# Optimization experiments

Hardware: AMD Instinct MI355X
Metric: run time of the kernel (lower is better)

The kernel has to match this reference:

```python
import jax, jax.numpy as jnp
import numpy as np

H = 8
D = 512
DK = D // H  # 64
ALPHA = 0.2  # leaky relu negative slope


def setup_inputs() -> dict:
    key = jax.random.key(0)
    ks = jax.random.split(key, 10)
    B, N = 8, 1024
    query = jax.random.normal(ks[0], (B, N, D), dtype=jnp.float32)
    key_t = jax.random.normal(ks[1], (B, N, D), dtype=jnp.float32)
    value = jax.random.normal(ks[2], (B, N, D), dtype=jnp.float32)
    mask = jax.random.randint(ks[3], (B, N, N), 0, 2, dtype=jnp.int32)
    scale = 0.02
    Wq = jax.random.normal(ks[4], (D, D), dtype=jnp.float32) * scale
    Wk = jax.random.normal(ks[5], (D, D), dtype=jnp.float32) * scale
    Wv = jax.random.normal(ks[6], (D, D), dtype=jnp.float32) * scale
    Wo = jax.random.normal(ks[7], (D, D), dtype=jnp.float32) * scale
    bq = jnp.zeros((D,), jnp.float32)
    bk = jnp.zeros((D,), jnp.float32)
    bv = jnp.zeros((D,), jnp.float32)
    bo = jnp.zeros((D,), jnp.float32)
    # xavier-uniform-like init for the attention vector a: shape (h, 2*d_k)
    limit = float(np.sqrt(6.0 / (H + 2 * DK)))
    a = jax.random.uniform(ks[8], (H, 2 * DK), dtype=jnp.float32, minval=-limit, maxval=limit)
    return {"query": query, "key": key_t, "value": value, "mask": mask,
            "Wq": Wq, "bq": bq, "Wk": Wk, "bk": bk, "Wv": Wv, "bv": bv,
            "Wo": Wo, "bo": bo, "a": a}


def reference(query, key, value, mask, Wq, bq, Wk, bk, Wv, bv, Wo, bo, a):
    B, N, _ = query.shape

    def proj(x, W, b):
        # torch Linear: x @ W.T + b, then split heads -> (B, H, N, DK)
        return (x @ W.T + b).reshape(B, N, H, DK).transpose(0, 2, 1, 3)

    q = proj(query, Wq, bq)
    k = proj(key, Wk, bk)
    v = proj(value, Wv, bv)

    # 'cat' attention: scores[b,h,i,j] = concat(q_i, k_j) . a[h]
    #                = q_i . a[h,:DK] + k_j . a[h,DK:]  (algebraic decomposition,
    #                 avoids the O(N^2 * 2*DK) concat tensor of the torch code)
    sq = jnp.einsum('bhnd,hd->bhn', q, a[:, :DK])
    sk = jnp.einsum('bhnd,hd->bhn', k, a[:, DK:])
    scores = sq[:, :, :, None] + sk[:, :, None, :]  # (B, H, N, N)

    # mask == 0 -> -inf (mask broadcast over heads), applied BEFORE leaky relu
    scores = jnp.where(mask[:, None, :, :] == 0, -jnp.inf, scores)
    # leaky relu (leaky_relu(-inf) == -inf, preserved)
    scores = jnp.where(scores >= 0, scores, ALPHA * scores)

    p = jax.nn.softmax(scores, axis=-1)
    # fully-masked rows produce NaN -> replace with 0 (as in the torch code)
    p = jnp.where(jnp.isnan(p), jnp.zeros_like(p), p)

    x = jnp.einsum('bhnm,bhmd->bhnd', p, v)
    x = x.transpose(0, 2, 1, 3).reshape(B, N, D)
    return x @ Wo.T + bo
```

## Files before the change

### kernel.cpp

```cpp
#include <hip/hip_runtime.h>
#include <hip/hip_bf16.h>
#include <stdint.h>


typedef __attribute__((ext_vector_type(8))) short short8;
typedef __attribute__((ext_vector_type(4))) float f32x4;

#define LB __launch_bounds__(256)

union U8 { unsigned u[4]; short8 s; uint4 v; };
union U2 { unsigned u[2]; uint2 v; };

__device__ __forceinline__ unsigned short f2bf(float f) {
  unsigned int u = __float_as_uint(f);
  u += 0x7fffu + ((u >> 16) & 1u);
  return (unsigned short)(u >> 16);
}

__device__ __forceinline__ unsigned cvt_pk(float a, float b) {
  unsigned r;
  asm("v_cvt_pk_bf16_f32 %0, %1, %2" : "=v"(r) : "v"(a), "v"(b));
  return r;
}

__device__ __forceinline__ void async_cp16(const void* g, void* l) {
  __builtin_amdgcn_global_load_lds(
      (const __attribute__((address_space(1))) unsigned int*)g,
      (__attribute__((address_space(3))) unsigned int*)l, 16, 0, 0);
}

__global__ LB void prep_kernel(const int* __restrict__ mask, unsigned int* __restrict__ bits,
                               const float* __restrict__ value, unsigned short* __restrict__ vb,
                               const float* __restrict__ Wv, const float* __restrict__ Wo,
                               unsigned short* __restrict__ wv16, unsigned short* __restrict__ wo16,
                               const float* __restrict__ Wq, const float* __restrict__ Wk,
                               const float* __restrict__ a, const float* __restrict__ bq,
                               const float* __restrict__ bk,
                               unsigned short* __restrict__ Bfrag, float* __restrict__ qkb) {
  const int blk = blockIdx.x;
  if (blk < 32768) {
    const size_t idx = (size_t)blk * 256 + threadIdx.x;
    const unsigned long long bl = __ballot(mask[idx] != 0);
    if ((threadIdx.x & 63) == 0) {
      bits[idx >> 5] = (unsigned int)bl;
      bits[(idx >> 5) + 1] = (unsigned int)(bl >> 32);
    }
    return;
  }
  if (blk < 36864) {
    const int idx = ((blk - 32768) * 256 + threadIdx.x) * 4;
    const float4 v = *(const float4*)(value + idx);
    U2 pk;
    pk.u[0] = cvt_pk(v.x, v.y);
    pk.u[1] = cvt_pk(v.z, v.w);
    *(uint2*)(vb + idx) = pk.v;
    return;
  }
  if (blk < 37376) {
    const int wblk = blk - 36864;
    const float* src = wblk < 256 ? Wv : Wo;
    unsigned short* dst = wblk < 256 ? wv16 : wo16;
    const int idx = ((wblk & 255) * 256 + threadIdx.x) * 4;
    const float4 v = *(const float4*)(src + idx);
    U2 pk;
    pk.u[0] = cvt_pk(v.x, v.y);
    pk.u[1] = cvt_pk(v.z, v.w);
    *(uint2*)(dst + idx) = pk.v;
    return;
  }
  const int t = (blk - 37376) * 256 + threadIdx.x;
  const int d = t & 511, h = t >> 9;
  float aq = 0.f, ak = 0.f;
#pragma unroll 4
  for (int dk = 0; dk < 64; ++dk) {
    aq += Wq[(size_t)(h * 64 + dk) * 512 + d] * a[h * 128 + dk];
    ak += Wk[(size_t)(h * 64 + dk) * 512 + d] * a[h * 128 + 64 + dk];
  }
  const float L2E = 1.4426950408889634f;
  const int ks = d >> 5, lch = (d >> 3) & 3, tt = d & 7;
  Bfrag[((ks * 64 + (lch << 4) + h) << 3) + tt] = f2bf(aq * L2E);
  Bfrag[((ks * 64 + (lch << 4) + 8 + h) << 3) + tt] = f2bf(ak * L2E);
  if (d == 0) {
    float s1 = 0.f, s2 = 0.f;
    for (int dk = 0; dk < 64; ++dk) {
      s1 += bq[h * 64 + dk] * a[h * 128 + dk];
      s2 += bk[h * 64 + dk] * a[h * 128 + 64 + dk];
    }
    qkb[h] = s1 * L2E;
    qkb[8 + h] = s2 * L2E;
  }
}

__global__ LB void sqsk_kernel(const float* __restrict__ query, const float* __restrict__ key,
                               const unsigned short* __restrict__ Bfrag,
                               const float* __restrict__ qkb,
                               float* __restrict__ sq, float* __restrict__ sk) {
  __shared__ float comb[3 * 64 * 9];
  const int tid = threadIdx.x, wv = tid >> 6, l = tid & 63;
  const int m0 = blockIdx.x * 16;
  const int k0 = wv * 128;
  short8 bf[4];
#pragma unroll
  for (int ks = 0; ks < 4; ++ks)
    bf[ks] = *(const short8*)(Bfrag + (((wv * 4 + ks) * 64 + l) << 3));
  const float* qbase = query + (size_t)(m0 + (l & 15)) * 512 + k0 + ((l >> 4) << 3);
  const float* kbase = key + (size_t)(m0 + (l & 15)) * 512 + k0 + ((l >> 4) << 3);
  f32x4 cq = {}, ck = {};
#pragma unroll
  for (int ks = 0; ks < 4; ++ks) {
    const float4 q0 = *(const float4*)(qbase + ks * 32);
    const float4 q1 = *(const float4*)(qbase + ks * 32 + 4);
    const float4 k0v = *(const float4*)(kbase + ks * 32);
    const float4 k1v = *(const float4*)(kbase + ks * 32 + 4);
    U8 aq, ak;
    aq.u[0] = cvt_pk(q0.x, q0.y); aq.u[1] = cvt_pk(q0.z, q0.w);
    aq.u[2] = cvt_pk(q1.x, q1.y); aq.u[3] = cvt_pk(q1.z, q1.w);
    ak.u[0] = cvt_pk(k0v.x, k0v.y); ak.u[1] = cvt_pk(k0v.z, k0v.w);
    ak.u[2] = cvt_pk(k1v.x, k1v.y); ak.u[3] = cvt_pk(k1v.z, k1v.w);
    cq = __builtin_amdgcn_mfma_f32_16x16x32_bf16(aq.s, bf[ks], cq, 0, 0, 0);
    ck = __builtin_amdgcn_mfma_f32_16x16x32_bf16(ak.s, bf[ks], ck, 0, 0, 0);
  }
  if (wv) {
    float* p = comb + ((wv - 1) * 64 + l) * 9;
#pragma unroll
    for (int r = 0; r < 4; ++r) { p[r] = cq[r]; p[4 + r] = ck[r]; }
  }
  __syncthreads();
  if (wv == 0) {
#pragma unroll
    for (int j = 0; j < 3; ++j) {
      const float* p = comb + (j * 64 + l) * 9;
#pragma unroll
      for (int r = 0; r < 4; ++r) { cq[r] += p[r]; ck[r] += p[4 + r]; }
    }
    const int col = l & 15;
    const int mbase = m0 + ((l >> 4) << 2);
    const int b = mbase >> 10;
    const float bia = qkb[col];
    if (col < 8) {
      float* out = sq + ((size_t)b * 8 + col) * 1024;
#pragma unroll
      for (int r = 0; r < 4; ++r) out[(mbase + r) & 1023] = cq[r] + bia;
    } else {
      float* out = sk + ((size_t)b * 8 + (col - 8)) * 1024;
#pragma unroll
      for (int r = 0; r < 4; ++r) out[(mbase + r) & 1023] = ck[r] + bia;
    }
  }
}

template <int BB16, int MODE>
__global__ LB void gemm_bt(const unsigned short* __restrict__ A,
                           const void* __restrict__ Bwp,
                           const float* __restrict__ bias, void* __restrict__ outp) {
  __shared__ unsigned short As[2][32 * 32];
  __shared__ unsigned short Bs[2][128 * 32];
  const int tid = threadIdx.x;
  const int w = tid >> 6, l = tid & 63;
  const int lr = l & 15, lc = l >> 4;
  const int bm = blockIdx.x >> 2, bn = blockIdx.x & 3;
  const int m0 = bm * 32, n0 = bn * 128;
  const int wr = (w & 1) * 16, wc = (w >> 1) * 64;
  const int rch = (lc ^ ((lr >> 1) & 3)) << 3;
  const int arow = (w << 3) + (l >> 2);
  const int asc = (l & 3) ^ ((arow >> 1) & 3);
  const unsigned short* asrc = A + (size_t)(m0 + arow) * 512 + (asc << 3);
  const int crow = l >> 2;
  const unsigned short* b16 = (const unsigned short*)Bwp;
  const float* b32 = (const float*)Bwp;
  const int brow0 = (w << 4) + crow, brow1 = ((w + 4) << 4) + crow;
  const unsigned short* bsrc0 = b16 + (size_t)(n0 + brow0) * 512 + (((l & 3) ^ ((brow0 >> 1) & 3)) << 3);
  const unsigned short* bsrc1 = b16 + (size_t)(n0 + brow1) * 512 + (((l & 3) ^ ((brow1 >> 1) & 3)) << 3);

  f32x4 acc[4] = {};
  if (BB16) {
    if (l < 32) async_cp16(asrc, As[0] + (w << 8));
    async_cp16(bsrc0, Bs[0] + (w << 9));
    async_cp16(bsrc1, Bs[0] + ((w + 4) << 9));
    int buf = 0;
    for (int kt = 0; kt < 16; ++kt) {
      if (kt < 15) {
        const int k1 = (kt + 1) * 32;
        if (l < 32) async_cp16(asrc + k1, As[buf ^ 1] + (w << 8));
        async_cp16(bsrc0 + k1, Bs[buf ^ 1] + (w << 9));
        async_cp16(bsrc1 + k1, Bs[buf ^ 1] + ((w + 4) << 9));
        asm volatile("s_waitcnt vmcnt(3)" ::: "memory");
      } else {
        asm volatile("s_waitcnt vmcnt(0)" ::: "memory");
      }
      __builtin_amdgcn_sched_barrier(0);
      __builtin_amdgcn_s_barrier();
      const short8 af = *(const short8*)(As[buf] + (wr + lr) * 32 + rch);
      __builtin_amdgcn_s_setprio(1);
#pragma unroll
      for (int j = 0; j < 4; ++j) {
        const short8 bfr = *(const short8*)(Bs[buf] + (wc + j * 16 + lr) * 32 + rch);
        acc[j] = __builtin_amdgcn_mfma_f32_16x16x32_bf16(af, bfr, acc[j], 0, 0, 0);
      }
      __builtin_amdgcn_s_setprio(0);
      if (kt < 15) __builtin_amdgcn_s_barrier();
      buf ^= 1;
    }
  } else {
    for (int kt = 0; kt < 16; ++kt) {
      const int k0 = kt * 32;
      if (kt) __syncthreads();
      if (l < 32) async_cp16(asrc + k0, As[0] + (w << 8));
#pragma unroll
      for (int it = 0; it < 2; ++it) {
        const int idx = it * 256 + tid;
        const int row = idx >> 2, gr = idx & 3;
        const int sch = (gr ^ ((row >> 1) & 3)) << 3;
        const float4* src = (const float4*)(b32 + (size_t)(n0 + row) * 512 + k0 + gr * 8);
        const float4 b0 = src[0], b1 = src[1];
        U8 t8;
        t8.u[0] = cvt_pk(b0.x, b0.y); t8.u[1] = cvt_pk(b0.z, b0.w);
        t8.u[2] = cvt_pk(b1.x, b1.y); t8.u[3] = cvt_pk(b1.z, b1.w);
        *(uint4*)(Bs[0] + row * 32 + sch) = t8.v;
      }
      __syncthreads();
      const short8 af = *(const short8*)(As[0] + (wr + lr) * 32 + rch);
#pragma unroll
      for (int j = 0; j < 4; ++j) {
        const short8 bfr = *(const short8*)(Bs[0] + (wc + j * 16 + lr) * 32 + rch);
        acc[j] = __builtin_amdgcn_mfma_f32_16x16x32_bf16(af, bfr, acc[j], 0, 0, 0);
      }
    }
  }
#pragma unroll
  for (int j = 0; j < 4; ++j) {
    const int nn = n0 + wc + j * 16 + lr;
    const float bia = bias[nn];
    const int mm0 = m0 + wr + lc * 4;
    if (MODE == 0) {
      float* out = (float*)outp;
#pragma unroll
      for (int r = 0; r < 4; ++r)
        out[(size_t)(mm0 + r) * 512 + nn] = acc[j][r] + bia;
    } else {
      unsigned short* out = (unsigned short*)outp;
      const int b = mm0 >> 10, t0 = mm0 & 1023;
      const int h = nn >> 6, dk = nn & 63;
      U2 pk;
      pk.u[0] = cvt_pk(acc[j][0] + bia, acc[j][1] + bia);
      pk.u[1] = cvt_pk(acc[j][2] + bia, acc[j][3] + bia);
      *(uint2*)(out + (((size_t)((b * 8 + h) * 64 + dk)) << 10) + t0) = pk.v;
    }
  }
}

__global__ LB void attn_kernel(const float* __restrict__ sq, const float* __restrict__ sk,
                               const unsigned char* __restrict__ mbits,
                               const unsigned short* __restrict__ vt,
                               unsigned short* __restrict__ xb) {
  __shared__ char smem[28672];
  unsigned short* vts = (unsigned short*)smem;
  float* sks = (float*)(smem + 16384);
  char* mks = smem + 20480;
  const int tid = threadIdx.x;
  const int w = tid >> 6, l = tid & 63;
  const int lr = l & 15, lc = l >> 4;
  const int bid = blockIdx.x;
  const int bh = bid >> 4, iblk = bid & 15;
  const int b = bh >> 3, h = bh & 7;
  const int i0b = iblk * 64;
  const float* sqp = sq + (size_t)bh * 1024;
  const float* skp = sk + (size_t)bh * 1024;
  const unsigned short* vtp = vt + ((size_t)bh << 16);
  const unsigned char* mrow = mbits + ((size_t)b << 17);

  async_cp16(skp + (w << 8) + l * 4, sks + (w << 8));
#pragma unroll
  for (int m = 0; m < 2; ++m) {
    const int row = (w << 4) + (m << 3) + (l >> 3);
    const int c = (l & 7) ^ (row & 7);
    async_cp16(mrow + (size_t)(i0b + row) * 128 + (c << 4), mks + (w << 11) + (m << 10));
  }
  const int strow = (w << 4) + (l >> 2);
  const int stc = (l & 3) ^ ((strow >> 1) & 3);
  const unsigned short* srcw = vtp + strow * 1024 + (stc << 3);
  async_cp16(srcw, vts + (w << 9));
  async_cp16(srcw + 32, vts + 2048 + (w << 9));

  const int rowl = (w << 4) + lr;
  const float sq1 = sqp[i0b + rowl];
  __syncthreads();

  f32x4 acc[4] = {};
  f32x4 accs = {};
  short8 ones;
#pragma unroll
  for (int t = 0; t < 8; ++t) ones[t] = (short)0x3f80;
  const int mrowbase = rowl << 7;
  const int rxorb = (rowl & 7) << 4;
  const int vread = (lc ^ ((lr >> 1) & 3)) << 3;

  int bufp = 0;
  for (int it = 0; it < 16; ++it) {
    if (it < 15) {
      const int sl = (it + 1) << 1;
      unsigned short* dst = vts + ((bufp ^ 1) << 12) + (w << 9);
      async_cp16(srcw + sl * 32, dst);
      async_cp16(srcw + sl * 32 + 32, dst + 2048);
      asm volatile("s_waitcnt vmcnt(2)" ::: "memory");
    } else {
      asm volatile("s_waitcnt vmcnt(0)" ::: "memory");
    }
    __builtin_amdgcn_sched_barrier(0);
    __builtin_amdgcn_s_barrier();
#pragma unroll
    for (int sub = 0; sub < 2; ++sub) {
      const int jb = (it << 6) + (sub << 5);
      const unsigned int mb = (unsigned char)mks[mrowbase + (((jb >> 3) + lc) ^ rxorb)];
      const f32x4 s0 = *(const f32x4*)(sks + jb + (lc << 3));
      const f32x4 s1 = *(const f32x4*)(sks + jb + (lc << 3) + 4);
      float e[8];
#pragma unroll
      for (int t = 0; t < 8; ++t) {
        float s = sq1 + (t < 4 ? s0[t] : s1[t - 4]);
        s = fmaxf(s, 0.2f * s);
        const float ex = __builtin_amdgcn_exp2f(s);
        e[t] = (mb & (1u << t)) ? ex : 0.0f;
      }
      U8 pa;
      pa.u[0] = cvt_pk(e[0], e[1]); pa.u[1] = cvt_pk(e[2], e[3]);
      pa.u[2] = cvt_pk(e[4], e[5]); pa.u[3] = cvt_pk(e[6], e[7]);
      const unsigned short* vb_base = vts + (bufp << 12) + (sub << 11) + vread;
      __builtin_amdgcn_s_setprio(1);
#pragma unroll
      for (int c = 0; c < 4; ++c) {
        const short8 bv = *(const short8*)(vb_base + ((c << 4) + lr) * 32);
        acc[c] = __builtin_amdgcn_mfma_f32_16x16x32_bf16(pa.s, bv, acc[c], 0, 0, 0);
      }
      accs = __builtin_amdgcn_mfma_f32_16x16x32_bf16(pa.s, ones, accs, 0, 0, 0);
      __builtin_amdgcn_s_setprio(0);
    }
    if (it < 15) __builtin_amdgcn_s_barrier();
    bufp ^= 1;
  }

#pragma unroll
  for (int r = 0; r < 4; ++r) {
    const float s = accs[r];
    const float inv = s > 0.0f ? 1.0f / s : 0.0f;
    const int i = i0b + (w << 4) + lc * 4 + r;
#pragma unroll
    for (int c = 0; c < 4; ++c)
      xb[(((size_t)(b * 1024 + i)) << 9) + h * 64 + c * 16 + lr] =
          f2bf(acc[c][r] * inv);
  }
}

extern "C" void kernel_launch(void* const* d_in, const int* in_sizes, int n_in,
                              void* d_out, int out_size, void* d_ws, size_t ws_size,
                              hipStream_t stream) {
  const float* query = (const float*)d_in[0];
  const float* key   = (const float*)d_in[1];
  const float* value = (const float*)d_in[2];
  const int*   mask  = (const int*)d_in[3];
  const float* Wq = (const float*)d_in[4];
  const float* bq = (const float*)d_in[5];
  const float* Wk = (const float*)d_in[6];
  const float* bk = (const float*)d_in[7];
  const float* Wv = (const float*)d_in[8];
  const float* bv = (const float*)d_in[9];
  const float* Wo = (const float*)d_in[10];
  const float* bo = (const float*)d_in[11];
  const float* a  = (const float*)d_in[12];

  char* oc = (char*)d_out;
  unsigned short* vt = (unsigned short*)(oc + 0);
  unsigned int* mbits = (unsigned int*)(oc + 8388608);
  float* sqv = (float*)(oc + 9437184);
  float* skv = (float*)(oc + 9699328);
  unsigned short* Bfrag = (unsigned short*)(oc + 9961472);
  float* qkb = (float*)(oc + 9977856);
  unsigned short* wv16 = (unsigned short*)(oc + 10485760);
  unsigned short* wo16f = (unsigned short*)(oc + 11010048);
  unsigned short* vb = (unsigned short*)d_ws;
  unsigned short* xb = (unsigned short*)d_ws;

  const bool roomy = ws_size >= 8912896;
  unsigned short* wo16 = roomy ? (unsigned short*)((char*)d_ws + 8388608) : wo16f;

  prep_kernel<<<37392, 256, 0, stream>>>(mask, mbits, value, vb, Wv, Wo, wv16, wo16,
                                         Wq, Wk, a, bq, bk, Bfrag, qkb);
  sqsk_kernel<<<512, 256, 0, stream>>>(query, key, Bfrag, qkb, sqv, skv);
  gemm_bt<1, 1><<<1024, 256, 0, stream>>>(vb, (const void*)wv16, bv, (void*)vt);
  attn_kernel<<<1024, 256, 0, stream>>>(sqv, skv, (const unsigned char*)mbits, vt, xb);
  if (roomy)
    gemm_bt<1, 0><<<1024, 256, 0, stream>>>(xb, (const void*)wo16, bo, d_out);
  else
    gemm_bt<0, 0><<<1024, 256, 0, stream>>>(xb, (const void*)Wo, bo, d_out);
}
```

Before: 90.43 us.

## Vectorize mask packing, merge sqsk with V GEMM, double attention row tile

The mask bit-packing now has each thread read four ints with one vector load and builds the bit words through shared memory, so it needs a quarter of the blocks. The sq/sk projection kernel and the V projection GEMM are merged into one launch with disjoint block ranges, removing a kernel launch and letting the two run concurrently. The attention kernel now handles 128 query rows per block instead of 64, with two row groups per wave, so each staged V tile is reused twice. This halves the attention grid and raises LDS use, which may reduce occupancy.

```diff
diff --git a/kernel.cpp b/kernel.cpp
--- a/kernel.cpp
+++ b/kernel.cpp
@@ -37,18 +37,24 @@
                                const float* __restrict__ a, const float* __restrict__ bq,
                                const float* __restrict__ bk,
                                unsigned short* __restrict__ Bfrag, float* __restrict__ qkb) {
-  const int blk = blockIdx.x;
-  if (blk < 32768) {
-    const size_t idx = (size_t)blk * 256 + threadIdx.x;
-    const unsigned long long bl = __ballot(mask[idx] != 0);
-    if ((threadIdx.x & 63) == 0) {
-      bits[idx >> 5] = (unsigned int)bl;
-      bits[(idx >> 5) + 1] = (unsigned int)(bl >> 32);
+  const int blk = blockIdx.x, tid = threadIdx.x;
+  if (blk < 8192) {
+    __shared__ unsigned char nb[256];
+    const size_t e0 = ((size_t)blk * 256 + tid) * 4;
+    const int4 m = *(const int4*)(mask + e0);
+    nb[tid] = (unsigned char)((m.x != 0) | ((m.y != 0) << 1) | ((m.z != 0) << 2) | ((m.w != 0) << 3));
+    __syncthreads();
+    if (tid < 32) {
+      const uint2 p = *(const uint2*)(nb + tid * 8);
+      const unsigned lo = p.x, hi = p.y;
+      const unsigned wl = (lo & 0xFu) | ((lo >> 4) & 0xF0u) | ((lo >> 8) & 0xF00u) | ((lo >> 12) & 0xF000u);
+      const unsigned wh = (hi & 0xFu) | ((hi >> 4) & 0xF0u) | ((hi >> 8) & 0xF00u) | ((hi >> 12) & 0xF000u);
+      bits[blk * 32 + tid] = wl | (wh << 16);
     }
     return;
   }
-  if (blk < 36864) {
-    const int idx = ((blk - 32768) * 256 + threadIdx.x) * 4;
+  if (blk < 12288) {
+    const int idx = ((blk - 8192) * 256 + tid) * 4;
     const float4 v = *(const float4*)(value + idx);
     U2 pk;
     pk.u[0] = cvt_pk(v.x, v.y);
@@ -56,11 +62,11 @@
     *(uint2*)(vb + idx) = pk.v;
     return;
   }
-  if (blk < 37376) {
-    const int wblk = blk - 36864;
+  if (blk < 12800) {
+    const int wblk = blk - 12288;
     const float* src = wblk < 256 ? Wv : Wo;
     unsigned short* dst = wblk < 256 ? wv16 : wo16;
-    const int idx = ((wblk & 255) * 256 + threadIdx.x) * 4;
+    const int idx = ((wblk & 255) * 256 + tid) * 4;
     const float4 v = *(const float4*)(src + idx);
     U2 pk;
     pk.u[0] = cvt_pk(v.x, v.y);
@@ -68,7 +74,7 @@
     *(uint2*)(dst + idx) = pk.v;
     return;
   }
-  const int t = (blk - 37376) * 256 + threadIdx.x;
+  const int t = (blk - 12800) * 256 + tid;
   const int d = t & 511, h = t >> 9;
   float aq = 0.f, ak = 0.f;
 #pragma unroll 4
@@ -91,61 +97,124 @@
   }
 }
 
-__global__ LB void sqsk_kernel(const float* __restrict__ query, const float* __restrict__ key,
-                               const unsigned short* __restrict__ Bfrag,
-                               const float* __restrict__ qkb,
-                               float* __restrict__ sq, float* __restrict__ sk) {
-  __shared__ float comb[3 * 64 * 9];
-  const int tid = threadIdx.x, wv = tid >> 6, l = tid & 63;
-  const int m0 = blockIdx.x * 16;
-  const int k0 = wv * 128;
-  short8 bf[4];
-#pragma unroll
-  for (int ks = 0; ks < 4; ++ks)
-    bf[ks] = *(const short8*)(Bfrag + (((wv * 4 + ks) * 64 + l) << 3));
-  const float* qbase = query + (size_t)(m0 + (l & 15)) * 512 + k0 + ((l >> 4) << 3);
-  const float* kbase = key + (size_t)(m0 + (l & 15)) * 512 + k0 + ((l >> 4) << 3);
-  f32x4 cq = {}, ck = {};
-#pragma unroll
-  for (int ks = 0; ks < 4; ++ks) {
-    const float4 q0 = *(const float4*)(qbase + ks * 32);
-    const float4 q1 = *(const float4*)(qbase + ks * 32 + 4);
-    const float4 k0v = *(const float4*)(kbase + ks * 32);
-    const float4 k1v = *(const float4*)(kbase + ks * 32 + 4);
-    U8 aq, ak;
-    aq.u[0] = cvt_pk(q0.x, q0.y); aq.u[1] = cvt_pk(q0.z, q0.w);
-    aq.u[2] = cvt_pk(q1.x, q1.y); aq.u[3] = cvt_pk(q1.z, q1.w);
-    ak.u[0] = cvt_pk(k0v.x, k0v.y); ak.u[1] = cvt_pk(k0v.z, k0v.w);
-    ak.u[2] = cvt_pk(k1v.x, k1v.y); ak.u[3] = cvt_pk(k1v.z, k1v.w);
-    cq = __builtin_amdgcn_mfma_f32_16x16x32_bf16(aq.s, bf[ks], cq, 0, 0, 0);
-    ck = __builtin_amdgcn_mfma_f32_16x16x32_bf16(ak.s, bf[ks], ck, 0, 0, 0);
-  }
-  if (wv) {
-    float* p = comb + ((wv - 1) * 64 + l) * 9;
-#pragma unroll
-    for (int r = 0; r < 4; ++r) { p[r] = cq[r]; p[4 + r] = ck[r]; }
-  }
-  __syncthreads();
-  if (wv == 0) {
-#pragma unroll
-    for (int j = 0; j < 3; ++j) {
-      const float* p = comb + (j * 64 + l) * 9;
-#pragma unroll
-      for (int r = 0; r < 4; ++r) { cq[r] += p[r]; ck[r] += p[4 + r]; }
-    }
-    const int col = l & 15;
-    const int mbase = m0 + ((l >> 4) << 2);
-    const int b = mbase >> 10;
-    const float bia = qkb[col];
-    if (col < 8) {
-      float* out = sq + ((size_t)b * 8 + col) * 1024;
-#pragma unroll
-      for (int r = 0; r < 4; ++r) out[(mbase + r) & 1023] = cq[r] + bia;
+__global__ LB void sqsk_gemmv_kernel(const float* __restrict__ query, const float* __restrict__ key,
+                                     const unsigned short* __restrict__ Bfrag,
+                                     const float* __restrict__ qkb,
+                                     float* __restrict__ sq, float* __restrict__ sk,
+                                     const unsigned short* __restrict__ vbA,
+                                     const unsigned short* __restrict__ wv16,
+                                     const float* __restrict__ bvb,
+                                     unsigned short* __restrict__ vt) {
+  __shared__ char sm[20480];
+  const int tid = threadIdx.x, w = tid >> 6, l = tid & 63;
+  const int lr = l & 15, lc = l >> 4;
+  if (blockIdx.x < 512) {
+    float* comb = (float*)sm;
+    const int m0 = blockIdx.x * 16;
+    const int k0 = w * 128;
+    short8 bf[4];
+#pragma unroll
+    for (int ks = 0; ks < 4; ++ks)
+      bf[ks] = *(const short8*)(Bfrag + (((w * 4 + ks) * 64 + l) << 3));
+    const float* qbase = query + (size_t)(m0 + lr) * 512 + k0 + (lc << 3);
+    const float* kbase = key + (size_t)(m0 + lr) * 512 + k0 + (lc << 3);
+    f32x4 cq = {}, ck = {};
+#pragma unroll
+    for (int ks = 0; ks < 4; ++ks) {
+      const float4 q0 = *(const float4*)(qbase + ks * 32);
+      const float4 q1 = *(const float4*)(qbase + ks * 32 + 4);
+      const float4 k0v = *(const float4*)(kbase + ks * 32);
+      const float4 k1v = *(const float4*)(kbase + ks * 32 + 4);
+      U8 aq, ak;
+      aq.u[0] = cvt_pk(q0.x, q0.y); aq.u[1] = cvt_pk(q0.z, q0.w);
+      aq.u[2] = cvt_pk(q1.x, q1.y); aq.u[3] = cvt_pk(q1.z, q1.w);
+      ak.u[0] = cvt_pk(k0v.x, k0v.y); ak.u[1] = cvt_pk(k0v.z, k0v.w);
+      ak.u[2] = cvt_pk(k1v.x, k1v.y); ak.u[3] = cvt_pk(k1v.z, k1v.w);
+      cq = __builtin_amdgcn_mfma_f32_16x16x32_bf16(aq.s, bf[ks], cq, 0, 0, 0);
+      ck = __builtin_amdgcn_mfma_f32_16x16x32_bf16(ak.s, bf[ks], ck, 0, 0, 0);
+    }
+    if (w) {
+      float* p = comb + ((w - 1) * 64 + l) * 9;
+#pragma unroll
+      for (int r = 0; r < 4; ++r) { p[r] = cq[r]; p[4 + r] = ck[r]; }
+    }
+    __syncthreads();
+    if (w == 0) {
+#pragma unroll
+      for (int j = 0; j < 3; ++j) {
+        const float* p = comb + (j * 64 + l) * 9;
+#pragma unroll
+        for (int r = 0; r < 4; ++r) { cq[r] += p[r]; ck[r] += p[4 + r]; }
+      }
+      const int col = l & 15;
+      const int mbase = m0 + (lc << 2);
+      const int b = mbase >> 10;
+      const float bia = qkb[col];
+      if (col < 8) {
+        float* out = sq + ((size_t)b * 8 + col) * 1024;
+#pragma unroll
+        for (int r = 0; r < 4; ++r) out[(mbase + r) & 1023] = cq[r] + bia;
+      } else {
+        float* out = sk + ((size_t)b * 8 + (col - 8)) * 1024;
+#pragma unroll
+        for (int r = 0; r < 4; ++r) out[(mbase + r) & 1023] = ck[r] + bia;
+      }
+    }
+    return;
+  }
+  unsigned short* As = (unsigned short*)sm;
+  unsigned short* Bs = (unsigned short*)(sm + 4096);
+  const int bid = blockIdx.x - 512;
+  const int bm = bid >> 2, bn = bid & 3;
+  const int m0 = bm * 32, n0 = bn * 128;
+  const int wr = (w & 1) * 16, wc = (w >> 1) * 64;
+  const int rch = (lc ^ ((lr >> 1) & 3)) << 3;
+  const int arow = (w << 3) + (l >> 2);
+  const int asc = (l & 3) ^ ((arow >> 1) & 3);
+  const unsigned short* asrc = vbA + (size_t)(m0 + arow) * 512 + (asc << 3);
+  const int crow = l >> 2;
+  const int brow0 = (w << 4) + crow, brow1 = ((w + 4) << 4) + crow;
+  const unsigned short* bsrc0 = wv16 + (size_t)(n0 + brow0) * 512 + (((l & 3) ^ ((brow0 >> 1) & 3)) << 3);
+  const unsigned short* bsrc1 = wv16 + (size_t)(n0 + brow1) * 512 + (((l & 3) ^ ((brow1 >> 1) & 3)) << 3);
+  f32x4 acc[4] = {};
+  if (l < 32) async_cp16(asrc, As + (w << 8));
+  async_cp16(bsrc0, Bs + (w << 9));
+  async_cp16(bsrc1, Bs + ((w + 4) << 9));
+  int buf = 0;
+  for (int kt = 0; kt < 16; ++kt) {
+    if (kt < 15) {
+      const int k1 = (kt + 1) * 32;
+      if (l < 32) async_cp16(asrc + k1, As + ((buf ^ 1) << 10) + (w << 8));
+      async_cp16(bsrc0 + k1, Bs + ((buf ^ 1) << 12) + (w << 9));
+      async_cp16(bsrc1 + k1, Bs + ((buf ^ 1) << 12) + ((w + 4) << 9));
+      asm volatile("s_waitcnt vmcnt(3)" ::: "memory");
     } else {
-      float* out = sk + ((size_t)b * 8 + (col - 8)) * 1024;
-#pragma unroll
-      for (int r = 0; r < 4; ++r) out[(mbase + r) & 1023] = ck[r] + bia;
-    }
+      asm volatile("s_waitcnt vmcnt(0)" ::: "memory");
+    }
+    __builtin_amdgcn_sched_barrier(0);
+    __builtin_amdgcn_s_barrier();
+    const short8 af = *(const short8*)(As + (buf << 10) + (wr + lr) * 32 + rch);
+    __builtin_amdgcn_s_setprio(1);
+#pragma unroll
+    for (int j = 0; j < 4; ++j) {
+      const short8 bfr = *(const short8*)(Bs + (buf << 12) + (wc + j * 16 + lr) * 32 + rch);
+      acc[j] = __builtin_amdgcn_mfma_f32_16x16x32_bf16(af, bfr, acc[j], 0, 0, 0);
+    }
+    __builtin_amdgcn_s_setprio(0);
+    if (kt < 15) __builtin_amdgcn_s_barrier();
+    buf ^= 1;
+  }
+#pragma unroll
+  for (int j = 0; j < 4; ++j) {
+    const int nn = n0 + wc + j * 16 + lr;
+    const float bia = bvb[nn];
+    const int mm0 = m0 + wr + lc * 4;
+    const int b = mm0 >> 10, t0 = mm0 & 1023;
+    const int h = nn >> 6, dk = nn & 63;
+    U2 pk;
+    pk.u[0] = cvt_pk(acc[j][0] + bia, acc[j][1] + bia);
+    pk.u[1] = cvt_pk(acc[j][2] + bia, acc[j][3] + bia);
+    *(uint2*)(vt + (((size_t)((b * 8 + h) * 64 + dk)) << 10) + t0) = pk.v;
   }
 }
 
@@ -253,17 +322,17 @@
                                const unsigned char* __restrict__ mbits,
                                const unsigned short* __restrict__ vt,
                                unsigned short* __restrict__ xb) {
-  __shared__ char smem[28672];
+  __shared__ char smem[53248];
   unsigned short* vts = (unsigned short*)smem;
-  float* sks = (float*)(smem + 16384);
-  char* mks = smem + 20480;
+  float* sks = (float*)(smem + 32768);
+  char* mks = smem + 36864;
   const int tid = threadIdx.x;
   const int w = tid >> 6, l = tid & 63;
   const int lr = l & 15, lc = l >> 4;
   const int bid = blockIdx.x;
-  const int bh = bid >> 4, iblk = bid & 15;
+  const int bh = bid & 63, iblk = bid >> 6;
   const int b = bh >> 3, h = bh & 7;
-  const int i0b = iblk * 64;
+  const int i0b = iblk << 7;
   const float* sqp = sq + (size_t)bh * 1024;
   const float* skp = sk + (size_t)bh * 1024;
   const unsigned short* vtp = vt + ((size_t)bh << 16);
@@ -271,83 +340,100 @@
 
   async_cp16(skp + (w << 8) + l * 4, sks + (w << 8));
 #pragma unroll
-  for (int m = 0; m < 2; ++m) {
-    const int row = (w << 4) + (m << 3) + (l >> 3);
+  for (int m = 0; m < 4; ++m) {
+    const int row = (w << 5) + (m << 3) + (l >> 3);
     const int c = (l & 7) ^ (row & 7);
-    async_cp16(mrow + (size_t)(i0b + row) * 128 + (c << 4), mks + (w << 11) + (m << 10));
-  }
-  const int strow = (w << 4) + (l >> 2);
-  const int stc = (l & 3) ^ ((strow >> 1) & 3);
-  const unsigned short* srcw = vtp + strow * 1024 + (stc << 3);
-  async_cp16(srcw, vts + (w << 9));
-  async_cp16(srcw + 32, vts + 2048 + (w << 9));
-
-  const int rowl = (w << 4) + lr;
-  const float sq1 = sqp[i0b + rowl];
+    async_cp16(mrow + (size_t)(i0b + row) * 128 + (c << 4), mks + (w << 12) + (m << 10));
+  }
+  const int stl = l >> 2;
+  const int stc = (l & 3) ^ ((stl >> 1) & 3);
+#define STAGE_VTS(tb, jb)                                                      \
+  {                                                                            \
+    unsigned short* dst = vts + ((tb) << 13) + (w << 11);                      \
+    const unsigned short* s_ = vtp + stl * 1024 + (jb) + (w << 5) + (stc << 3);\
+    async_cp16(s_, dst);                                                       \
+    async_cp16(s_ + 16384, dst + 512);                                         \
+    async_cp16(s_ + 32768, dst + 1024);                                        \
+    async_cp16(s_ + 49152, dst + 1536);                                        \
+  }
+  STAGE_VTS(0, 0);
+  float sq2[2];
+#pragma unroll
+  for (int g = 0; g < 2; ++g) sq2[g] = sqp[i0b + (w << 5) + (g << 4) + lr];
   __syncthreads();
 
-  f32x4 acc[4] = {};
-  f32x4 accs = {};
+  f32x4 acc[2][4] = {};
+  f32x4 accs[2] = {};
   short8 ones;
 #pragma unroll
   for (int t = 0; t < 8; ++t) ones[t] = (short)0x3f80;
-  const int mrowbase = rowl << 7;
-  const int rxorb = (rowl & 7) << 4;
   const int vread = (lc ^ ((lr >> 1) & 3)) << 3;
-
-  int bufp = 0;
-  for (int it = 0; it < 16; ++it) {
-    if (it < 15) {
-      const int sl = (it + 1) << 1;
-      unsigned short* dst = vts + ((bufp ^ 1) << 12) + (w << 9);
-      async_cp16(srcw + sl * 32, dst);
-      async_cp16(srcw + sl * 32 + 32, dst + 2048);
-      asm volatile("s_waitcnt vmcnt(2)" ::: "memory");
+  const int rx = (lr & 7) << 4;
+
+  int tb = 0;
+  for (int it = 0; it < 8; ++it) {
+    if (it < 7) {
+      STAGE_VTS(tb ^ 1, (it + 1) << 7);
+      asm volatile("s_waitcnt vmcnt(4)" ::: "memory");
     } else {
       asm volatile("s_waitcnt vmcnt(0)" ::: "memory");
     }
     __builtin_amdgcn_sched_barrier(0);
     __builtin_amdgcn_s_barrier();
 #pragma unroll
-    for (int sub = 0; sub < 2; ++sub) {
-      const int jb = (it << 6) + (sub << 5);
-      const unsigned int mb = (unsigned char)mks[mrowbase + (((jb >> 3) + lc) ^ rxorb)];
+    for (int s = 0; s < 4; ++s) {
+      const int jb = (it << 7) + (s << 5);
+      const int qb = (jb >> 3) + lc;
       const f32x4 s0 = *(const f32x4*)(sks + jb + (lc << 3));
       const f32x4 s1 = *(const f32x4*)(sks + jb + (lc << 3) + 4);
-      float e[8];
-#pragma unroll
-      for (int t = 0; t < 8; ++t) {
-        float s = sq1 + (t < 4 ? s0[t] : s1[t - 4]);
-        s = fmaxf(s, 0.2f * s);
-        const float ex = __builtin_amdgcn_exp2f(s);
-        e[t] = (mb & (1u << t)) ? ex : 0.0f;
-      }
-      U8 pa;
-      pa.u[0] = cvt_pk(e[0], e[1]); pa.u[1] = cvt_pk(e[2], e[3]);
-      pa.u[2] = cvt_pk(e[4], e[5]); pa.u[3] = cvt_pk(e[6], e[7]);
-      const unsigned short* vb_base = vts + (bufp << 12) + (sub << 11) + vread;
+      U8 pa[2];
+#pragma unroll
+      for (int g = 0; g < 2; ++g) {
+        const int rowl = (w << 5) + (g << 4) + lr;
+        const unsigned mb = (unsigned char)mks[(rowl << 7) + (qb ^ rx)];
+        const float sqv = sq2[g];
+        float e[8];
+#pragma unroll
+        for (int t = 0; t < 8; ++t) {
+          float sv = sqv + (t < 4 ? s0[t] : s1[t - 4]);
+          sv = fmaxf(sv, 0.2f * sv);
+          const float ex = __builtin_amdgcn_exp2f(sv);
+          e[t] = (mb & (1u << t)) ? ex : 0.0f;
+        }
+        pa[g].u[0] = cvt_pk(e[0], e[1]); pa[g].u[1] = cvt_pk(e[2], e[3]);
+        pa[g].u[2] = cvt_pk(e[4], e[5]); pa[g].u[3] = cvt_pk(e[6], e[7]);
+      }
+      const unsigned short* vbb = vts + (tb << 13) + (s << 11) + vread;
       __builtin_amdgcn_s_setprio(1);
 #pragma unroll
       for (int c = 0; c < 4; ++c) {
-        const short8 bv = *(const short8*)(vb_base + ((c << 4) + lr) * 32);
-        acc[c] = __builtin_amdgcn_mfma_f32_16x16x32_bf16(pa.s, bv, acc[c], 0, 0, 0);
-      }
-      accs = __builtin_amdgcn_mfma_f32_16x16x32_bf16(pa.s, ones, accs, 0, 0, 0);
+        const short8 bv = *(const short8*)(vbb + ((c << 4) + lr) * 32);
+#pragma unroll
+        for (int g = 0; g < 2; ++g)
+          acc[g][c] = __builtin_amdgcn_mfma_f32_16x16x32_bf16(pa[g].s, bv, acc[g][c], 0, 0, 0);
+      }
+#pragma unroll
+      for (int g = 0; g < 2; ++g)
+        accs[g] = __builtin_amdgcn_mfma_f32_16x16x32_bf16(pa[g].s, ones, accs[g], 0, 0, 0);
       __builtin_amdgcn_s_setprio(0);
     }
-    if (it < 15) __builtin_amdgcn_s_barrier();
-    bufp ^= 1;
-  }
-
-#pragma unroll
-  for (int r = 0; r < 4; ++r) {
-    const float s = accs[r];
-    const float inv = s > 0.0f ? 1.0f / s : 0.0f;
-    const int i = i0b + (w << 4) + lc * 4 + r;
-#pragma unroll
-    for (int c = 0; c < 4; ++c)
-      xb[(((size_t)(b * 1024 + i)) << 9) + h * 64 + c * 16 + lr] =
-          f2bf(acc[c][r] * inv);
+    if (it < 7) __builtin_amdgcn_s_barrier();
+    tb ^= 1;
+  }
+#undef STAGE_VTS
+
+#pragma unroll
+  for (int g = 0; g < 2; ++g) {
+#pragma unroll
+    for (int r = 0; r < 4; ++r) {
+      const float sv = accs[g][r];
+      const float inv = sv > 0.0f ? 1.0f / sv : 0.0f;
+      const int i = i0b + (w << 5) + (g << 4) + (lc << 2) + r;
+#pragma unroll
+      for (int c = 0; c < 4; ++c)
+        xb[(((size_t)(b * 1024 + i)) << 9) + h * 64 + (c << 4) + lr] =
+            f2bf(acc[g][c][r] * inv);
+    }
   }
 }
 
@@ -383,11 +469,11 @@
   const bool roomy = ws_size >= 8912896;
   unsigned short* wo16 = roomy ? (unsigned short*)((char*)d_ws + 8388608) : wo16f;
 
-  prep_kernel<<<37392, 256, 0, stream>>>(mask, mbits, value, vb, Wv, Wo, wv16, wo16,
+  prep_kernel<<<12816, 256, 0, stream>>>(mask, mbits, value, vb, Wv, Wo, wv16, wo16,
                                          Wq, Wk, a, bq, bk, Bfrag, qkb);
-  sqsk_kernel<<<512, 256, 0, stream>>>(query, key, Bfrag, qkb, sqv, skv);
-  gemm_bt<1, 1><<<1024, 256, 0, stream>>>(vb, (const void*)wv16, bv, (void*)vt);
-  attn_kernel<<<1024, 256, 0, stream>>>(sqv, skv, (const unsigned char*)mbits, vt, xb);
+  sqsk_gemmv_kernel<<<1536, 256, 0, stream>>>(query, key, Bfrag, qkb, sqv, skv,
+                                              vb, wv16, bv, vt);
+  attn_kernel<<<512, 256, 0, stream>>>(sqv, skv, (const unsigned char*)mbits, vt, xb);
   if (roomy)
     gemm_bt<1, 0><<<1024, 256, 0, stream>>>(xb, (const void*)wo16, bo, d_out);
   else
```

Measured after the change: 82.15 us. 9.2% less time.
